# Performance work log

Hardware: AMD Instinct MI355X
Metric: run time of the kernel (lower is better)

Reference implementation:

```python
import jax, jax.numpy as jnp
import numpy as np

B, T, E, H = 2, 1024, 1024, 16
HD = E // H
TEMP = 0.5


def setup_inputs() -> dict:
    key = jax.random.key(0)
    ks = jax.random.split(key, 20)
    d = {
        "query1": jax.random.normal(ks[0], (B, T, E), jnp.float32),
        "query2": jax.random.normal(ks[1], (B, T, E), jnp.float32),
        "key": jax.random.normal(ks[2], (B, T, E), jnp.float32),
        "value": jax.random.normal(ks[3], (B, T, E), jnp.float32),
    }
    s = 1.0 / np.sqrt(E)
    names = ["Wq", "Wq2", "Wq3", "Wk", "Wv", "Wo"]
    for i, n in enumerate(names):
        d[n] = jax.random.normal(ks[4 + i], (E, E), jnp.float32) * s
        d["b" + n[1:]] = jax.random.normal(ks[10 + i], (E,), jnp.float32) * 0.01
    return d


def _heads(x):
    # [B,T,E] -> [B,H,T,HD]
    b, t, _ = x.shape
    return x.reshape(b, t, H, HD).transpose(0, 2, 1, 3)


def reference(query1, query2, key, value,
              Wq, bq, Wq2, bq2, Wq3, bq3, Wk, bk, Wv, bv, Wo, bo):
    q = _heads(query1 @ Wq.T + bq)
    q2 = _heads(query2 @ Wq2.T + bq2)
    q3 = _heads(key @ Wq3.T + bq3)
    k = _heads(key @ Wk.T + bk)
    v = _heads(value @ Wv.T + bv)
    b, _, t, _ = q.shape
    scale = 1.0 / np.sqrt(HD)

    def global_attn(qx):
        s = jnp.einsum('bhtd,bhsd->bhts', qx, k) * scale  # [B,H,T,T]
        # global softmax over flattened T*T, temperature-scaled, times T
        a = jax.nn.softmax((s / TEMP).reshape(b, H, t * t), axis=-1)
        return a.reshape(b, H, t, t) * t

    a1 = global_attn(q)
    a2 = global_attn(q2)
    a3 = global_attn(q3)
    attn_out = jnp.einsum('bhts,bhsd->bthd', (a1 + a2 + a3) / 3.0, v)
    attn_out = attn_out.reshape(b, t, E)
    output = attn_out @ Wo.T + bo
    return output, a1
```

## Files before the change

kernel.cpp:

```cpp
#include <hip/hip_runtime.h>
#include <hip/hip_bf16.h>


#define B_ 2
#define T_ 1024
#define E_ 1024
#define H_ 16
#define HD_ 64
#define BH_ 32

#define CEXP 0.36067376022224085f

typedef float f32x4 __attribute__((ext_vector_type(4)));
typedef short bfrag __attribute__((ext_vector_type(8)));

__device__ __forceinline__ unsigned short f2b(float f) {
  unsigned int u = __float_as_uint(f);
  u += 0x7fffu + ((u >> 16) & 1u);
  return (unsigned short)(u >> 16);
}

__device__ __forceinline__ void gl_lds16(const unsigned short* g, unsigned short* l) {
  __builtin_amdgcn_global_load_lds(
      reinterpret_cast<const __attribute__((address_space(1))) unsigned int*>(
          reinterpret_cast<uintptr_t>(g)),
      reinterpret_cast<__attribute__((address_space(3))) unsigned int*>(
          reinterpret_cast<uintptr_t>(l)),
      16, 0, 0);
}

struct CvtArgs { const float* src[10]; unsigned short* dst[10]; int n[10]; };

__global__ __launch_bounds__(256) void cvt_kernel(CvtArgs a) {
  const int z = blockIdx.y;
  const float* __restrict__ s = a.src[z];
  unsigned short* __restrict__ d = a.dst[z];
  const int n = a.n[z];
  const int stride = gridDim.x * 256 * 4;
  for (int i = (blockIdx.x * 256 + threadIdx.x) * 4; i < n; i += stride) {
    float4 v = *(const float4*)(s + i);
    ushort4 o;
    o.x = f2b(v.x); o.y = f2b(v.y); o.z = f2b(v.z); o.w = f2b(v.w);
    *(ushort4*)(d + i) = o;
  }
}

__device__ __forceinline__ void mm128_core(const unsigned short* __restrict__ A,
                                           const unsigned short* __restrict__ W,
                                           int m0, int n0,
                                           unsigned short* As, unsigned short* Bs,
                                           f32x4 acc[4][4]) {
  const int tid  = threadIdx.x;
  const int lane = tid & 63, w = tid >> 6;
  const int lrow = lane & 15, quad = lane >> 4;
  const int wm = (w >> 1) * 64, wn = (w & 1) * 64;
  const int srow = tid >> 2, soff = (tid & 3) * 8;

  const unsigned short* Ar0 = A + (size_t)(m0 + srow) * E_ + soff;
  const unsigned short* Ar1 = Ar0 + (size_t)64 * E_;
  const unsigned short* Br0 = W + (size_t)(n0 + srow) * E_ + soff;
  const unsigned short* Br1 = Br0 + (size_t)64 * E_;
  unsigned short* Ad0 = As + tid * 8;
  unsigned short* Ad1 = As + 2048 + tid * 8;
  unsigned short* Bd0 = Bs + tid * 8;
  unsigned short* Bd1 = Bs + 2048 + tid * 8;

  for (int k0 = 0; k0 < E_; k0 += 32) {
    __syncthreads();
    gl_lds16(Ar0 + k0, Ad0);
    gl_lds16(Ar1 + k0, Ad1);
    gl_lds16(Br0 + k0, Bd0);
    gl_lds16(Br1 + k0, Bd1);
    __syncthreads();
    bfrag af[4], bf_[4];
#pragma unroll
    for (int mt = 0; mt < 4; mt++)
      af[mt] = *(const bfrag*)(As + (wm + mt * 16 + lrow) * 32 + quad * 8);
#pragma unroll
    for (int nt = 0; nt < 4; nt++)
      bf_[nt] = *(const bfrag*)(Bs + (wn + nt * 16 + lrow) * 32 + quad * 8);
#pragma unroll
    for (int mt = 0; mt < 4; mt++)
#pragma unroll
      for (int nt = 0; nt < 4; nt++)
        acc[mt][nt] = __builtin_amdgcn_mfma_f32_16x16x32_bf16(af[mt], bf_[nt], acc[mt][nt], 0, 0, 0);
  }
}

struct ProjArgs {
  const unsigned short* X[5];
  const unsigned short* W[5];
  const float* bias[5];
  unsigned short* dst[5];
};

__global__ __launch_bounds__(256) void proj_kernel(ProjArgs pa) {
  __shared__ unsigned short As[128 * 32];
  __shared__ unsigned short Bs[128 * 32];
  const int z = blockIdx.z;
  const int m0 = blockIdx.y * 128, n0 = blockIdx.x * 128;
  f32x4 acc[4][4];
#pragma unroll
  for (int mt = 0; mt < 4; mt++)
#pragma unroll
    for (int nt = 0; nt < 4; nt++) acc[mt][nt] = (f32x4)0.f;

  mm128_core(pa.X[z], pa.W[z], m0, n0, As, Bs, acc);

  const int tid = threadIdx.x, lane = tid & 63, w = tid >> 6;
  const int lrow = lane & 15, quad = lane >> 4;
  const int wm = (w >> 1) * 64, wn = (w & 1) * 64;
  const float* __restrict__ bias = pa.bias[z];
  unsigned short* __restrict__ dst = pa.dst[z];
  float bv[4];
#pragma unroll
  for (int nt = 0; nt < 4; nt++) bv[nt] = bias[n0 + wn + nt * 16 + lrow];
#pragma unroll
  for (int mt = 0; mt < 4; mt++)
#pragma unroll
    for (int nt = 0; nt < 4; nt++)
#pragma unroll
      for (int ii = 0; ii < 4; ii++) {
        const int m = m0 + wm + mt * 16 + quad * 4 + ii;
        const int n = n0 + wn + nt * 16 + lrow;
        const float v = acc[mt][nt][ii] + bv[nt];
        const int b = m >> 10, t = m & 1023, h = n >> 6, dd = n & 63;
        size_t idx;
        if (z == 4)
          idx = ((size_t)((b * H_ + h) * HD_ + dd)) * T_ + t;
        else
          idx = ((size_t)((b * H_ + h) * T_ + t)) * HD_ + dd;
        dst[idx] = f2b(v);
      }
}

__global__ __launch_bounds__(256) void attn_sums_kernel(
    const unsigned short* __restrict__ Q1, const unsigned short* __restrict__ Q2,
    const unsigned short* __restrict__ Q3, const unsigned short* __restrict__ Kh,
    float* __restrict__ sums) {
  const int flat = blockIdx.x + 8 * (blockIdx.y + 2 * blockIdx.z);
  const int swz  = (flat & 7) * 64 + (flat >> 3);
  const int bx   = swz & 7;
  const int shalf = (swz >> 3) & 1;
  const int bh   = swz >> 4;

  const int tid = threadIdx.x, lane = tid & 63, w = tid >> 6;
  const int lrow = lane & 15, quad = lane >> 4;
  const int tw = w >> 1, sw = w & 1;
  const int tb = bx * 128 + tw * 64;
  const int sbase = shalf * 512;
  const size_t base = (size_t)bh * T_ * HD_;
  const unsigned short* Qs[3] = {Q1 + base, Q2 + base, Q3 + base};
  const unsigned short* Kb = Kh + base;

  float ls[3][4];
#pragma unroll
  for (int i = 0; i < 3; i++)
#pragma unroll
    for (int ii = 0; ii < 4; ii++) ls[i][ii] = 0.f;

  for (int j = 0; j < 4; j++) {
    const int sb = sbase + j * 128 + sw * 64;
#pragma unroll
    for (int i = 0; i < 3; i++) {
      f32x4 acc[4][4];
#pragma unroll
      for (int mt = 0; mt < 4; mt++)
#pragma unroll
        for (int nt = 0; nt < 4; nt++) acc[mt][nt] = (f32x4)0.f;
#pragma unroll
      for (int kk = 0; kk < 2; kk++) {
        bfrag af[4], bf_[4];
#pragma unroll
        for (int mt = 0; mt < 4; mt++)
          af[mt] = *(const bfrag*)(Qs[i] + (size_t)(tb + mt * 16 + lrow) * HD_ + kk * 32 + quad * 8);
#pragma unroll
        for (int nt = 0; nt < 4; nt++)
          bf_[nt] = *(const bfrag*)(Kb + (size_t)(sb + nt * 16 + lrow) * HD_ + kk * 32 + quad * 8);
#pragma unroll
        for (int mt = 0; mt < 4; mt++)
#pragma unroll
          for (int nt = 0; nt < 4; nt++)
            acc[mt][nt] = __builtin_amdgcn_mfma_f32_16x16x32_bf16(af[mt], bf_[nt], acc[mt][nt], 0, 0, 0);
      }
#pragma unroll
      for (int mt = 0; mt < 4; mt++)
#pragma unroll
        for (int nt = 0; nt < 4; nt++)
#pragma unroll
          for (int ii = 0; ii < 4; ii++)
            ls[i][ii] += exp2f(acc[mt][nt][ii] * CEXP);
    }
  }
#pragma unroll
  for (int i = 0; i < 3; i++) {
    float v = (ls[i][0] + ls[i][1]) + (ls[i][2] + ls[i][3]);
    for (int off = 32; off > 0; off >>= 1) v += __shfl_down(v, off, 64);
    if (lane == 0) atomicAdd(&sums[i * BH_ + bh], v);
  }
}

__global__ __launch_bounds__(256) void attn_main_kernel(
    const unsigned short* __restrict__ Q1, const unsigned short* __restrict__ Q2,
    const unsigned short* __restrict__ Q3, const unsigned short* __restrict__ Kh,
    const unsigned short* __restrict__ Vt, const float* __restrict__ sums,
    float* __restrict__ a1out, unsigned short* __restrict__ attn_out) {
  __shared__ unsigned short P[128 * 136];
  const int flat = blockIdx.x + 8 * blockIdx.y;
  const int swz  = (flat & 7) * 32 + (flat >> 3);
  const int bx   = swz & 7;
  const int bh   = swz >> 3;

  const int tid = threadIdx.x, lane = tid & 63, w = tid >> 6;
  const int lrow = lane & 15, quad = lane >> 4;
  const int tw = w >> 1, sw = w & 1, dw = sw;
  const int b = bh >> 4, h = bh & 15;
  const int tb = bx * 128 + tw * 64;
  const size_t base = (size_t)bh * T_ * HD_;
  const unsigned short* Qs[3] = {Q1 + base, Q2 + base, Q3 + base};
  const unsigned short* Kb = Kh + base;
  const unsigned short* Vb = Vt + (size_t)bh * HD_ * T_;

  float r[3];
#pragma unroll
  for (int i = 0; i < 3; i++) r[i] = (float)T_ / (3.f * sums[i * BH_ + bh]);
  const float a1s = 3.f * r[0];

  f32x4 oacc[4][2];
#pragma unroll
  for (int mt = 0; mt < 4; mt++) { oacc[mt][0] = (f32x4)0.f; oacc[mt][1] = (f32x4)0.f; }

  for (int s0 = 0; s0 < T_; s0 += 128) {
    const int sb = s0 + sw * 64;
    f32x4 pc[4][4];
#pragma unroll
    for (int mt = 0; mt < 4; mt++)
#pragma unroll
      for (int nt = 0; nt < 4; nt++) pc[mt][nt] = (f32x4)0.f;

#pragma unroll
    for (int i = 0; i < 3; i++) {
      f32x4 acc[4][4];
#pragma unroll
      for (int mt = 0; mt < 4; mt++)
#pragma unroll
        for (int nt = 0; nt < 4; nt++) acc[mt][nt] = (f32x4)0.f;
#pragma unroll
      for (int kk = 0; kk < 2; kk++) {
        bfrag af[4], bf_[4];
#pragma unroll
        for (int mt = 0; mt < 4; mt++)
          af[mt] = *(const bfrag*)(Qs[i] + (size_t)(tb + mt * 16 + lrow) * HD_ + kk * 32 + quad * 8);
#pragma unroll
        for (int nt = 0; nt < 4; nt++)
          bf_[nt] = *(const bfrag*)(Kb + (size_t)(sb + nt * 16 + lrow) * HD_ + kk * 32 + quad * 8);
#pragma unroll
        for (int mt = 0; mt < 4; mt++)
#pragma unroll
          for (int nt = 0; nt < 4; nt++)
            acc[mt][nt] = __builtin_amdgcn_mfma_f32_16x16x32_bf16(af[mt], bf_[nt], acc[mt][nt], 0, 0, 0);
      }
      const float ri = r[i];
#pragma unroll
      for (int mt = 0; mt < 4; mt++)
#pragma unroll
        for (int nt = 0; nt < 4; nt++)
#pragma unroll
          for (int ii = 0; ii < 4; ii++) {
            const float e = exp2f(acc[mt][nt][ii] * CEXP);
            pc[mt][nt][ii] += ri * e;
            if (i == 0) {
              const int t = tb + mt * 16 + quad * 4 + ii;
              const int s = sb + nt * 16 + lrow;
              __builtin_nontemporal_store(e * a1s,
                  a1out + ((size_t)bh * T_ + t) * T_ + s);
            }
          }
    }
    __syncthreads();
#pragma unroll
    for (int mt = 0; mt < 4; mt++)
#pragma unroll
      for (int nt = 0; nt < 4; nt++)
#pragma unroll
        for (int ii = 0; ii < 4; ii++) {
          const int tl = tw * 64 + mt * 16 + quad * 4 + ii;
          const int sl = sw * 64 + nt * 16 + lrow;
          P[tl * 136 + sl] = f2b(pc[mt][nt][ii]);
        }
    __syncthreads();
#pragma unroll
    for (int kk = 0; kk < 4; kk++) {
      bfrag pf[4], vf[2];
#pragma unroll
      for (int mt = 0; mt < 4; mt++)
        pf[mt] = *(const bfrag*)(P + (tw * 64 + mt * 16 + lrow) * 136 + kk * 32 + quad * 8);
#pragma unroll
      for (int nt = 0; nt < 2; nt++)
        vf[nt] = *(const bfrag*)(Vb + (size_t)(dw * 32 + nt * 16 + lrow) * T_ + s0 + kk * 32 + quad * 8);
#pragma unroll
      for (int mt = 0; mt < 4; mt++)
#pragma unroll
        for (int nt = 0; nt < 2; nt++)
          oacc[mt][nt] = __builtin_amdgcn_mfma_f32_16x16x32_bf16(pf[mt], vf[nt], oacc[mt][nt], 0, 0, 0);
    }
  }
#pragma unroll
  for (int mt = 0; mt < 4; mt++)
#pragma unroll
    for (int nt = 0; nt < 2; nt++)
#pragma unroll
      for (int ii = 0; ii < 4; ii++) {
        const int t = tb + mt * 16 + quad * 4 + ii;
        const int dd = dw * 32 + nt * 16 + lrow;
        attn_out[((size_t)(b * T_ + t)) * E_ + h * HD_ + dd] = f2b(oacc[mt][nt][ii]);
      }
}

__global__ __launch_bounds__(256) void outproj_kernel(
    const unsigned short* __restrict__ Ab, const unsigned short* __restrict__ Wb,
    const float* __restrict__ bias, float* __restrict__ out) {
  __shared__ unsigned short As[128 * 32];
  __shared__ unsigned short Bs[128 * 32];
  const int m0 = blockIdx.y * 128, n0 = blockIdx.x * 128;
  f32x4 acc[4][4];
#pragma unroll
  for (int mt = 0; mt < 4; mt++)
#pragma unroll
    for (int nt = 0; nt < 4; nt++) acc[mt][nt] = (f32x4)0.f;

  mm128_core(Ab, Wb, m0, n0, As, Bs, acc);

  const int tid = threadIdx.x, lane = tid & 63, w = tid >> 6;
  const int lrow = lane & 15, quad = lane >> 4;
  const int wm = (w >> 1) * 64, wn = (w & 1) * 64;
  float bv[4];
#pragma unroll
  for (int nt = 0; nt < 4; nt++) bv[nt] = bias[n0 + wn + nt * 16 + lrow];
#pragma unroll
  for (int mt = 0; mt < 4; mt++)
#pragma unroll
    for (int nt = 0; nt < 4; nt++)
#pragma unroll
      for (int ii = 0; ii < 4; ii++) {
        const int m = m0 + wm + mt * 16 + quad * 4 + ii;
        const int n = n0 + wn + nt * 16 + lrow;
        out[(size_t)m * E_ + n] = acc[mt][nt][ii] + bv[nt];
      }
}

extern "C" void kernel_launch(void* const* d_in, const int* in_sizes, int n_in,
                              void* d_out, int out_size, void* d_ws, size_t ws_size,
                              hipStream_t stream) {
  const float* q1f  = (const float*)d_in[0];
  const float* q2f  = (const float*)d_in[1];
  const float* keyf = (const float*)d_in[2];
  const float* valf = (const float*)d_in[3];
  const float* Wq  = (const float*)d_in[4];  const float* bq  = (const float*)d_in[5];
  const float* Wq2 = (const float*)d_in[6];  const float* bq2 = (const float*)d_in[7];
  const float* Wq3 = (const float*)d_in[8];  const float* bq3 = (const float*)d_in[9];
  const float* Wk  = (const float*)d_in[10]; const float* bk  = (const float*)d_in[11];
  const float* Wv  = (const float*)d_in[12]; const float* bv  = (const float*)d_in[13];
  const float* Wo  = (const float*)d_in[14]; const float* bo  = (const float*)d_in[15];

  char* ws = (char*)d_ws;
  const size_t MB = 1024 * 1024;
  unsigned short* xq1  = (unsigned short*)(ws + 0 * MB);
  unsigned short* xq2  = (unsigned short*)(ws + 4 * MB);
  unsigned short* xkey = (unsigned short*)(ws + 8 * MB);
  unsigned short* xval = (unsigned short*)(ws + 12 * MB);
  unsigned short* wq   = (unsigned short*)(ws + 16 * MB);
  unsigned short* wq2  = (unsigned short*)(ws + 18 * MB);
  unsigned short* wq3  = (unsigned short*)(ws + 20 * MB);
  unsigned short* wk   = (unsigned short*)(ws + 22 * MB);
  unsigned short* wv   = (unsigned short*)(ws + 24 * MB);
  unsigned short* wo   = (unsigned short*)(ws + 26 * MB);
  unsigned short* Qh1  = (unsigned short*)(ws + 28 * MB);
  unsigned short* Qh2  = (unsigned short*)(ws + 32 * MB);
  unsigned short* Qh3  = (unsigned short*)(ws + 36 * MB);
  unsigned short* Kh   = (unsigned short*)(ws + 40 * MB);
  unsigned short* Vt   = (unsigned short*)(ws + 44 * MB);
  unsigned short* attn = (unsigned short*)(ws + 48 * MB);
  float* sums          = (float*)(ws + 52 * MB);

  CvtArgs ca;
  const float* srcs[10] = {q1f, q2f, keyf, valf, Wq, Wq2, Wq3, Wk, Wv, Wo};
  unsigned short* dsts[10] = {xq1, xq2, xkey, xval, wq, wq2, wq3, wk, wv, wo};
  for (int i = 0; i < 10; i++) { ca.src[i] = srcs[i]; ca.dst[i] = dsts[i]; ca.n[i] = (i < 4) ? 2097152 : 1048576; }
  cvt_kernel<<<dim3(2048, 10), 256, 0, stream>>>(ca);

  hipMemsetAsync(sums, 0, 3 * BH_ * sizeof(float), stream);

  ProjArgs pa;
  const unsigned short* Xs[5] = {xq1, xq2, xkey, xkey, xval};
  const unsigned short* Ws_[5] = {wq, wq2, wq3, wk, wv};
  const float* Bi[5] = {bq, bq2, bq3, bk, bv};
  unsigned short* Ds[5] = {Qh1, Qh2, Qh3, Kh, Vt};
  for (int i = 0; i < 5; i++) { pa.X[i] = Xs[i]; pa.W[i] = Ws_[i]; pa.bias[i] = Bi[i]; pa.dst[i] = Ds[i]; }
  proj_kernel<<<dim3(8, 16, 5), 256, 0, stream>>>(pa);

  attn_sums_kernel<<<dim3(8, 2, BH_), 256, 0, stream>>>(Qh1, Qh2, Qh3, Kh, sums);

  float* out = (float*)d_out;
  attn_main_kernel<<<dim3(8, BH_), 256, 0, stream>>>(Qh1, Qh2, Qh3, Kh, Vt, sums,
                                                     out + 2097152, attn);

  outproj_kernel<<<dim3(8, 16), 256, 0, stream>>>(attn, wo, bo, out);
}
```

Baseline: 394.7 us.

## Split attention key range across two blocks and fold partial sums into outproj GEMM

```diff
diff --git a/kernel.cpp b/kernel.cpp
--- a/kernel.cpp
+++ b/kernel.cpp
@@ -18,6 +18,12 @@
   unsigned int u = __float_as_uint(f);
   u += 0x7fffu + ((u >> 16) & 1u);
   return (unsigned short)(u >> 16);
+}
+
+__device__ __forceinline__ float fexp2(float x) {
+  float r;
+  asm("v_exp_f32 %0, %1" : "=v"(r) : "v"(x));
+  return r;
 }
 
 __device__ __forceinline__ void gl_lds16(const unsigned short* g, unsigned short* l) {
@@ -41,10 +47,17 @@
     float4 v = *(const float4*)(s + i);
     ushort4 o;
     o.x = f2b(v.x); o.y = f2b(v.y); o.z = f2b(v.z); o.w = f2b(v.w);
-    *(ushort4*)(d + i) = o;
+    if (z == 9) {
+      const int row = i >> 10, k = i & 1023;
+      *(ushort4*)(d + (size_t)row * 2048 + k) = o;
+      *(ushort4*)(d + (size_t)row * 2048 + 1024 + k) = o;
+    } else {
+      *(ushort4*)(d + i) = o;
+    }
   }
 }
 
+template <int KLEN>
 __device__ __forceinline__ void mm128_core(const unsigned short* __restrict__ A,
                                            const unsigned short* __restrict__ W,
                                            int m0, int n0,
@@ -56,16 +69,16 @@
   const int wm = (w >> 1) * 64, wn = (w & 1) * 64;
   const int srow = tid >> 2, soff = (tid & 3) * 8;
 
-  const unsigned short* Ar0 = A + (size_t)(m0 + srow) * E_ + soff;
-  const unsigned short* Ar1 = Ar0 + (size_t)64 * E_;
-  const unsigned short* Br0 = W + (size_t)(n0 + srow) * E_ + soff;
-  const unsigned short* Br1 = Br0 + (size_t)64 * E_;
+  const unsigned short* Ar0 = A + (size_t)(m0 + srow) * KLEN + soff;
+  const unsigned short* Ar1 = Ar0 + (size_t)64 * KLEN;
+  const unsigned short* Br0 = W + (size_t)(n0 + srow) * KLEN + soff;
+  const unsigned short* Br1 = Br0 + (size_t)64 * KLEN;
   unsigned short* Ad0 = As + tid * 8;
   unsigned short* Ad1 = As + 2048 + tid * 8;
   unsigned short* Bd0 = Bs + tid * 8;
   unsigned short* Bd1 = Bs + 2048 + tid * 8;
 
-  for (int k0 = 0; k0 < E_; k0 += 32) {
+  for (int k0 = 0; k0 < KLEN; k0 += 32) {
     __syncthreads();
     gl_lds16(Ar0 + k0, Ad0);
     gl_lds16(Ar1 + k0, Ad1);
@@ -105,7 +118,7 @@
 #pragma unroll
     for (int nt = 0; nt < 4; nt++) acc[mt][nt] = (f32x4)0.f;
 
-  mm128_core(pa.X[z], pa.W[z], m0, n0, As, Bs, acc);
+  mm128_core<E_>(pa.X[z], pa.W[z], m0, n0, As, Bs, acc);
 
   const int tid = threadIdx.x, lane = tid & 63, w = tid >> 6;
   const int lrow = lane & 15, quad = lane >> 4;
@@ -189,7 +202,7 @@
         for (int nt = 0; nt < 4; nt++)
 #pragma unroll
           for (int ii = 0; ii < 4; ii++)
-            ls[i][ii] += exp2f(acc[mt][nt][ii] * CEXP);
+            ls[i][ii] += fexp2(acc[mt][nt][ii] * CEXP);
     }
   }
 #pragma unroll
@@ -204,12 +217,13 @@
     const unsigned short* __restrict__ Q1, const unsigned short* __restrict__ Q2,
     const unsigned short* __restrict__ Q3, const unsigned short* __restrict__ Kh,
     const unsigned short* __restrict__ Vt, const float* __restrict__ sums,
-    float* __restrict__ a1out, unsigned short* __restrict__ attn_out) {
+    float* __restrict__ a1out, unsigned short* __restrict__ attn2) {
   __shared__ unsigned short P[128 * 136];
-  const int flat = blockIdx.x + 8 * blockIdx.y;
-  const int swz  = (flat & 7) * 32 + (flat >> 3);
+  const int flat = blockIdx.x + 8 * (blockIdx.y + 2 * blockIdx.z);
+  const int swz  = (flat & 7) * 64 + (flat >> 3);
   const int bx   = swz & 7;
-  const int bh   = swz >> 3;
+  const int sh   = (swz >> 3) & 1;
+  const int bh   = swz >> 4;
 
   const int tid = threadIdx.x, lane = tid & 63, w = tid >> 6;
   const int lrow = lane & 15, quad = lane >> 4;
@@ -230,7 +244,7 @@
 #pragma unroll
   for (int mt = 0; mt < 4; mt++) { oacc[mt][0] = (f32x4)0.f; oacc[mt][1] = (f32x4)0.f; }
 
-  for (int s0 = 0; s0 < T_; s0 += 128) {
+  for (int s0 = sh * 512; s0 < sh * 512 + 512; s0 += 128) {
     const int sb = s0 + sw * 64;
     f32x4 pc[4][4];
 #pragma unroll
@@ -267,7 +281,7 @@
         for (int nt = 0; nt < 4; nt++)
 #pragma unroll
           for (int ii = 0; ii < 4; ii++) {
-            const float e = exp2f(acc[mt][nt][ii] * CEXP);
+            const float e = fexp2(acc[mt][nt][ii] * CEXP);
             pc[mt][nt][ii] += ri * e;
             if (i == 0) {
               const int t = tb + mt * 16 + quad * 4 + ii;
@@ -313,12 +327,13 @@
       for (int ii = 0; ii < 4; ii++) {
         const int t = tb + mt * 16 + quad * 4 + ii;
         const int dd = dw * 32 + nt * 16 + lrow;
-        attn_out[((size_t)(b * T_ + t)) * E_ + h * HD_ + dd] = f2b(oacc[mt][nt][ii]);
+        attn2[((size_t)(b * T_ + t)) * 2048 + sh * 1024 + h * HD_ + dd] =
+            f2b(oacc[mt][nt][ii]);
       }
 }
 
 __global__ __launch_bounds__(256) void outproj_kernel(
-    const unsigned short* __restrict__ Ab, const unsigned short* __restrict__ Wb,
+    const unsigned short* __restrict__ A2, const unsigned short* __restrict__ W2,
     const float* __restrict__ bias, float* __restrict__ out) {
   __shared__ unsigned short As[128 * 32];
   __shared__ unsigned short Bs[128 * 32];
@@ -329,7 +344,7 @@
 #pragma unroll
     for (int nt = 0; nt < 4; nt++) acc[mt][nt] = (f32x4)0.f;
 
-  mm128_core(Ab, Wb, m0, n0, As, Bs, acc);
+  mm128_core<2048>(A2, W2, m0, n0, As, Bs, acc);
 
   const int tid = threadIdx.x, lane = tid & 63, w = tid >> 6;
   const int lrow = lane & 15, quad = lane >> 4;
@@ -374,18 +389,18 @@
   unsigned short* wq3  = (unsigned short*)(ws + 20 * MB);
   unsigned short* wk   = (unsigned short*)(ws + 22 * MB);
   unsigned short* wv   = (unsigned short*)(ws + 24 * MB);
-  unsigned short* wo   = (unsigned short*)(ws + 26 * MB);
   unsigned short* Qh1  = (unsigned short*)(ws + 28 * MB);
   unsigned short* Qh2  = (unsigned short*)(ws + 32 * MB);
   unsigned short* Qh3  = (unsigned short*)(ws + 36 * MB);
   unsigned short* Kh   = (unsigned short*)(ws + 40 * MB);
   unsigned short* Vt   = (unsigned short*)(ws + 44 * MB);
-  unsigned short* attn = (unsigned short*)(ws + 48 * MB);
-  float* sums          = (float*)(ws + 52 * MB);
+  unsigned short* attn2 = (unsigned short*)(ws + 48 * MB);
+  unsigned short* wo2   = (unsigned short*)(ws + 56 * MB);
+  float* sums           = (float*)(ws + 60 * MB);
 
   CvtArgs ca;
   const float* srcs[10] = {q1f, q2f, keyf, valf, Wq, Wq2, Wq3, Wk, Wv, Wo};
-  unsigned short* dsts[10] = {xq1, xq2, xkey, xval, wq, wq2, wq3, wk, wv, wo};
+  unsigned short* dsts[10] = {xq1, xq2, xkey, xval, wq, wq2, wq3, wk, wv, wo2};
   for (int i = 0; i < 10; i++) { ca.src[i] = srcs[i]; ca.dst[i] = dsts[i]; ca.n[i] = (i < 4) ? 2097152 : 1048576; }
   cvt_kernel<<<dim3(2048, 10), 256, 0, stream>>>(ca);
 
@@ -402,8 +417,8 @@
   attn_sums_kernel<<<dim3(8, 2, BH_), 256, 0, stream>>>(Qh1, Qh2, Qh3, Kh, sums);
 
   float* out = (float*)d_out;
-  attn_main_kernel<<<dim3(8, BH_), 256, 0, stream>>>(Qh1, Qh2, Qh3, Kh, Vt, sums,
-                                                     out + 2097152, attn);
-
-  outproj_kernel<<<dim3(8, 16), 256, 0, stream>>>(attn, wo, bo, out);
-}
+  attn_main_kernel<<<dim3(8, 2, BH_), 256, 0, stream>>>(Qh1, Qh2, Qh3, Kh, Vt, sums,
+                                                        out + 2097152, attn2);
+
+  outproj_kernel<<<dim3(8, 16), 256, 0, stream>>>(attn2, wo2, bo, out);
+}
```

Result: no change. 391.2 us (-0.9%).
